# Kernel optimization log

Hardware: AMD Instinct MI355X
Metric: run time of the kernel (lower is better)

## Reference

```python
import jax, jax.numpy as jnp
import numpy as np

NUM_HEADS = 8
SPLIT = 2  # split_size; idx=0 -> H_sp=H, W_sp=SPLIT (horizontal stripes)


def setup_inputs() -> dict:
    key = jax.random.key(0)
    k1, k2, k3 = jax.random.split(key, 3)
    B, C, H, W = 4, 64, 128, 128
    temp = jax.random.normal(k1, (B, 3, C, H, W), dtype=jnp.float32)
    conv_w = jax.random.normal(k2, (C, 1, 3, 3), dtype=jnp.float32) * 0.1  # depthwise OIHW
    conv_b = jax.random.normal(k3, (C,), dtype=jnp.float32) * 0.1
    return {"temp": temp, "conv_w": conv_w, "conv_b": conv_b}


def reference(temp, conv_w, conv_b):
    B, _, C, H, W = temp.shape
    hd = C // NUM_HEADS
    scale = hd ** (-0.5)
    H_sp, W_sp = H, SPLIT  # idx == 0

    # symmetric pad to multiples of window size (faithful to original; zero here)
    H_pad = (H_sp - H % H_sp) % H_sp
    W_pad = (W_sp - W % W_sp) % W_sp
    top, left = H_pad // 2, W_pad // 2
    x = jnp.pad(temp, ((0, 0), (0, 0), (0, 0), (top, H_pad - top), (left, W_pad - left)))
    H_, W_ = H + H_pad, W + W_pad
    q, k, v = x[:, 0], x[:, 1], x[:, 2]  # each [B,C,H_,W_]

    nW = (H_ // H_sp) * (W_ // W_sp)
    N = H_sp * W_sp  # tokens per window

    def im2cswin(t):
        # [B,C,H_,W_] -> [B*nW, heads, N, hd]
        w = t.reshape(B, C, H_ // H_sp, H_sp, W_ // W_sp, W_sp)
        w = w.transpose(0, 2, 4, 3, 5, 1).reshape(-1, N, C)
        return w.reshape(-1, N, NUM_HEADS, hd).transpose(0, 2, 1, 3)

    qh = im2cswin(q) * scale
    kh = im2cswin(k)

    # v windows as images [B*nW, C, H_sp, W_sp] for depthwise LePE conv
    vw = v.reshape(B, C, H_ // H_sp, H_sp, W_ // W_sp, W_sp)
    vw = vw.transpose(0, 2, 4, 1, 3, 5).reshape(-1, C, H_sp, W_sp)
    rpe = jax.lax.conv_general_dilated(
        vw, conv_w, window_strides=(1, 1), padding='SAME',
        feature_group_count=C, dimension_numbers=('NCHW', 'OIHW', 'NCHW'))
    rpe = rpe + conv_b[None, :, None, None]

    vh = vw.reshape(-1, NUM_HEADS, hd, N).transpose(0, 1, 3, 2)    # [B*nW,h,N,hd]
    rpeh = rpe.reshape(-1, NUM_HEADS, hd, N).transpose(0, 1, 3, 2)

    attn = jax.nn.softmax(jnp.einsum('whnd,whmd->whnm', qh, kh), axis=-1)
    out = jnp.einsum('whnm,whmd->whnd', attn, vh) + rpeh           # [B*nW,h,N,hd]

    out = out.transpose(0, 2, 1, 3).reshape(-1, N, C)              # [B*nW,N,C]
    # windows2img + crop
    out = out.reshape(B, H_ // H_sp, W_ // W_sp, H_sp, W_sp, C)
    out = out.transpose(0, 1, 3, 2, 4, 5).reshape(B, H_, W_, C)
    out = out[:, top:H + top, left:W + left, :]
    return out.reshape(B, H * W, C)
```

## Files before the change

kernel.cpp:

```cpp
#include <hip/hip_runtime.h>
#include <hip/hip_bf16.h>
#include <stdint.h>


typedef __attribute__((ext_vector_type(4))) short bf16x4;
typedef __attribute__((ext_vector_type(4))) float f32x4;

static __device__ __forceinline__ uint32_t pk2(float x, float y) {
    union { __hip_bfloat162 h2; uint32_t u; } c;
    c.h2 = __float22bfloat162_rn(make_float2(x, y));
    return c.u;
}
static __device__ __forceinline__ float bflo(uint32_t u){ return __uint_as_float(u<<16); }
static __device__ __forceinline__ float bfhi(uint32_t u){ return __uint_as_float(u & 0xffff0000u); }

static __device__ __forceinline__ uint2 ld2(const char* p) {
    uint2 r;
    r.x = *(const uint32_t*)(p);
    r.y = *(const uint32_t*)(p + 4);
    return r;
}

static __device__ __forceinline__ f32x4 mfma16x16x16bf16(bf16x4 a, bf16x4 b, f32x4 c) {
#if __has_builtin(__builtin_amdgcn_mfma_f32_16x16x16bf16_1k)
    return __builtin_amdgcn_mfma_f32_16x16x16bf16_1k(a, b, c, 0, 0, 0);
#else
    f32x4 d;
    asm volatile("v_mfma_f32_16x16x16_bf16 %0, %1, %2, %3\n\ts_nop 7\n\ts_nop 7"
                 : "=v"(d) : "v"(a), "v"(b), "v"(c));
    return d;
#endif
}

#define QK_TOK_STR 20
#define QK_WIN_STR 5120
#define V_CH_STR   536
#define V_WIN_STR  4288

__global__ __launch_bounds__(512, 4)
void lepe_attn(const float* __restrict__ temp,
               const float* __restrict__ conv_w,
               const float* __restrict__ conv_b,
               float* __restrict__ out)
{
    __shared__ __align__(16) char smem[58432];
    char* q_s = smem;
    char* k_s = smem + 20480;
    char* v_t = smem + 40960;
    float* cw_s = (float*)(smem + 58112);

    const int tid  = threadIdx.x;
    const int wave = tid >> 6, lane = tid & 63;
    const int lr = lane & 15, quad = lane >> 4;
    const int win   = wave & 3;
    const int qbase = (wave >> 2) * 8;

    const int bid = blockIdx.x;
    const int x  = bid & 7;
    int t_ = bid >> 3;
    const int wjh  = t_ & 1;  t_ >>= 1;
    const int head = t_ & 7;
    const int b    = t_ >> 3;
    const int wi   = x*8 + wjh*4 + win;

    const size_t cstr = 16384, sstr = 64 * cstr;
    const float qs = 0.35355339059327373f * 1.4426950408889634f;

    {
        const int cg = wave;
        const int hg = lane >> 1, hf1 = lane & 1;
        const int w0 = hf1 * 2;
        const float* bp = temp + (size_t)b*3*sstr + (size_t)(head*8 + cg)*cstr
                        + x*16 + wjh*8 + hf1*4;
        #pragma unroll
        for (int i = 0; i < 4; ++i) {
            int h = i*32 + hg;
            float4 fq = *(const float4*)(bp + (size_t)h*128);
            uint32_t a0 = pk2(fq.x*qs, fq.y*qs);
            uint32_t a1 = pk2(fq.z*qs, fq.w*qs);
            *(uint16_t*)(q_s + w0*QK_WIN_STR     + (2*h)*QK_TOK_STR   + cg*2) = (uint16_t)a0;
            *(uint16_t*)(q_s + w0*QK_WIN_STR     + (2*h+1)*QK_TOK_STR + cg*2) = (uint16_t)(a0>>16);
            *(uint16_t*)(q_s + (w0+1)*QK_WIN_STR + (2*h)*QK_TOK_STR   + cg*2) = (uint16_t)a1;
            *(uint16_t*)(q_s + (w0+1)*QK_WIN_STR + (2*h+1)*QK_TOK_STR + cg*2) = (uint16_t)(a1>>16);
            float4 fk = *(const float4*)(bp + sstr + (size_t)h*128);
            uint32_t b0 = pk2(fk.x, fk.y);
            uint32_t b1 = pk2(fk.z, fk.w);
            *(uint16_t*)(k_s + w0*QK_WIN_STR     + (2*h)*QK_TOK_STR   + cg*2) = (uint16_t)b0;
            *(uint16_t*)(k_s + w0*QK_WIN_STR     + (2*h+1)*QK_TOK_STR + cg*2) = (uint16_t)(b0>>16);
            *(uint16_t*)(k_s + (w0+1)*QK_WIN_STR + (2*h)*QK_TOK_STR   + cg*2) = (uint16_t)b1;
            *(uint16_t*)(k_s + (w0+1)*QK_WIN_STR + (2*h+1)*QK_TOK_STR + cg*2) = (uint16_t)(b1>>16);
            float4 fv = *(const float4*)(bp + 2*sstr + (size_t)h*128);
            *(uint32_t*)(v_t + w0*V_WIN_STR     + cg*V_CH_STR + 4*h + 4) = pk2(fv.x, fv.y);
            *(uint32_t*)(v_t + (w0+1)*V_WIN_STR + cg*V_CH_STR + 4*h + 4) = pk2(fv.z, fv.w);
        }
        if (tid < 72) cw_s[tid] = conv_w[head*72 + tid];
        if (tid < 8)  cw_s[72 + tid] = conv_b[head*8 + tid];
        if (tid < 32) {
            int vw = tid >> 3, vc = tid & 7;
            *(uint32_t*)(v_t + vw*V_WIN_STR + vc*V_CH_STR)       = 0;
            *(uint32_t*)(v_t + vw*V_WIN_STR + vc*V_CH_STR + 516) = 0;
        }
    }
    __syncthreads();

    const f32x4 zf = {0.f, 0.f, 0.f, 0.f};
    const uint2 z2 = make_uint2(0, 0);
    uint2 kf[16]; uint2 vf[16];
    #pragma unroll
    for (int T = 0; T < 16; ++T) {
        uint2 kk = ld2(k_s + win*QK_WIN_STR + (T*16 + lr)*QK_TOK_STR + (quad & 1)*8);
        kf[T] = (quad < 2) ? kk : z2;
        uint2 vv = ld2(v_t + win*V_WIN_STR + (lane & 7)*V_CH_STR + 4 + (T*16 + quad*4)*2);
        vf[T] = (lr < 8) ? vv : z2;
    }
    __syncthreads();

    {
        const int w2  = tid >> 7;
        const int chl = (tid >> 4) & 7;
        const int seg = tid & 15;
        const char* base = v_t + w2*V_WIN_STR + chl*V_CH_STR + seg*32;
        uint32_t d[10];
        *(uint2*)(d+0) = *(const uint2*)(base);
        *(uint2*)(d+2) = *(const uint2*)(base+8);
        *(uint2*)(d+4) = *(const uint2*)(base+16);
        *(uint2*)(d+6) = *(const uint2*)(base+24);
        *(uint2*)(d+8) = *(const uint2*)(base+32);
        float w9[9];
        #pragma unroll
        for (int k = 0; k < 9; ++k) w9[k] = cw_s[chl*9 + k];
        const float bia = cw_s[72 + chl];
        #pragma unroll
        for (int tt = 0; tt < 16; ++tt) {
            int tok = seg*16 + tt;
            int w01 = tok & 1;
            int L = (tt >> 1) * 2;
            float rp = bia;
            #pragma unroll
            for (int dy = 0; dy < 3; ++dy) {
                #pragma unroll
                for (int wp = 0; wp < 2; ++wp) {
                    int idx = L + 2*dy + wp;
                    uint32_t dw = d[idx >> 1];
                    float tap = (idx & 1) ? bfhi(dw) : bflo(dw);
                    rp = fmaf(w9[dy*3 + wp + 1 - w01], tap, rp);
                }
            }
            union { __hip_bfloat16 h; uint16_t u; } cv;
            cv.h = __float2bfloat16(rp);
            *(uint16_t*)(k_s + w2*QK_WIN_STR + tok*QK_TOK_STR + chl*2) = cv.u;
        }
    }
    __syncthreads();

    #pragma unroll 1
    for (int qg0 = 0; qg0 < 8; ++qg0) {
        const int qg = qbase + qg0;
        uint2 qq = ld2(q_s + win*QK_WIN_STR + (qg*16 + lr)*QK_TOK_STR + (quad & 1)*8);
        union { uint2 u; bf16x4 h4; } qf; qf.u = (quad < 2) ? qq : z2;
        f32x4 acc = zf;
        float rsum = 0.f;
        #pragma unroll
        for (int T = 0; T < 16; ++T) {
            union { uint2 u; bf16x4 h4; } kfu; kfu.u = kf[T];
            f32x4 sc = mfma16x16x16bf16(kfu.h4, qf.h4, zf);
            float e0 = __builtin_amdgcn_exp2f(sc[0]);
            float e1 = __builtin_amdgcn_exp2f(sc[1]);
            float e2 = __builtin_amdgcn_exp2f(sc[2]);
            float e3 = __builtin_amdgcn_exp2f(sc[3]);
            rsum += (e0 + e1) + (e2 + e3);
            union { uint2 u; bf16x4 h4; } pb; pb.u = make_uint2(pk2(e0,e1), pk2(e2,e3));
            union { uint2 u; bf16x4 h4; } vfu; vfu.u = vf[T];
            acc = mfma16x16x16bf16(vfu.h4, pb.h4, acc);
        }
        float rs = rsum;
        rs += __shfl_xor(rs, 16);
        rs += __shfl_xor(rs, 32);
        const float rinv = __builtin_amdgcn_rcpf(rs);
        if (quad < 2) {
            int tok = qg*16 + lr;
            int h = tok >> 1, w01 = tok & 1;
            uint2 rp2 = ld2(k_s + win*QK_WIN_STR + tok*QK_TOK_STR + quad*8);
            float4 ov;
            ov.x = fmaf(acc[0], rinv, bflo(rp2.x));
            ov.y = fmaf(acc[1], rinv, bfhi(rp2.x));
            ov.z = fmaf(acc[2], rinv, bflo(rp2.y));
            ov.w = fmaf(acc[3], rinv, bfhi(rp2.y));
            size_t addr = (size_t)b*1048576 + (size_t)(h*128 + wi*2 + w01)*64
                        + head*8 + quad*4;
            *(float4*)(out + addr) = ov;
        }
    }
}

extern "C" void kernel_launch(void* const* d_in, const int* in_sizes, int n_in,
                              void* d_out, int out_size, void* d_ws, size_t ws_size,
                              hipStream_t stream) {
    const float* temp = (const float*)d_in[0];
    const float* cw   = (const float*)d_in[1];
    const float* cb   = (const float*)d_in[2];
    float* o = (float*)d_out;
    (void)in_sizes; (void)n_in; (void)out_size; (void)d_ws; (void)ws_size;
    lepe_attn<<<dim3(512), dim3(512), 0, stream>>>(temp, cw, cb, o);
}
```

Before: 115.4 us.

## Shrink LDS with XOR-swizzled Q/K layout and fold softmax sum into MFMA

```diff
diff --git a/kernel.cpp b/kernel.cpp
--- a/kernel.cpp
+++ b/kernel.cpp
@@ -19,6 +19,10 @@
     r.x = *(const uint32_t*)(p);
     r.y = *(const uint32_t*)(p + 4);
     return r;
+}
+
+static __device__ __forceinline__ int qk_off(int tok) {
+    return (tok * 16) ^ ((tok >> 4 & 7) << 4);
 }
 
 static __device__ __forceinline__ f32x4 mfma16x16x16bf16(bf16x4 a, bf16x4 b, f32x4 c) {
@@ -32,22 +36,21 @@
 #endif
 }
 
-#define QK_TOK_STR 20
-#define QK_WIN_STR 5120
+#define QK_WIN_STR 4128
 #define V_CH_STR   536
 #define V_WIN_STR  4288
 
-__global__ __launch_bounds__(512, 4)
+__global__ __launch_bounds__(512, 6)
 void lepe_attn(const float* __restrict__ temp,
                const float* __restrict__ conv_w,
                const float* __restrict__ conv_b,
                float* __restrict__ out)
 {
-    __shared__ __align__(16) char smem[58432];
+    __shared__ __align__(16) char smem[50496];
     char* q_s = smem;
-    char* k_s = smem + 20480;
-    char* v_t = smem + 40960;
-    float* cw_s = (float*)(smem + 58112);
+    char* k_s = smem + 16512;
+    char* v_t = smem + 33024;
+    float* cw_s = (float*)(smem + 50176);
 
     const int tid  = threadIdx.x;
     const int wave = tid >> 6, lane = tid & 63;
@@ -75,20 +78,21 @@
         #pragma unroll
         for (int i = 0; i < 4; ++i) {
             int h = i*32 + hg;
+            int o0 = qk_off(2*h), o1 = qk_off(2*h + 1);
             float4 fq = *(const float4*)(bp + (size_t)h*128);
             uint32_t a0 = pk2(fq.x*qs, fq.y*qs);
             uint32_t a1 = pk2(fq.z*qs, fq.w*qs);
-            *(uint16_t*)(q_s + w0*QK_WIN_STR     + (2*h)*QK_TOK_STR   + cg*2) = (uint16_t)a0;
-            *(uint16_t*)(q_s + w0*QK_WIN_STR     + (2*h+1)*QK_TOK_STR + cg*2) = (uint16_t)(a0>>16);
-            *(uint16_t*)(q_s + (w0+1)*QK_WIN_STR + (2*h)*QK_TOK_STR   + cg*2) = (uint16_t)a1;
-            *(uint16_t*)(q_s + (w0+1)*QK_WIN_STR + (2*h+1)*QK_TOK_STR + cg*2) = (uint16_t)(a1>>16);
+            *(uint16_t*)(q_s + w0*QK_WIN_STR     + o0 + cg*2) = (uint16_t)a0;
+            *(uint16_t*)(q_s + w0*QK_WIN_STR     + o1 + cg*2) = (uint16_t)(a0>>16);
+            *(uint16_t*)(q_s + (w0+1)*QK_WIN_STR + o0 + cg*2) = (uint16_t)a1;
+            *(uint16_t*)(q_s + (w0+1)*QK_WIN_STR + o1 + cg*2) = (uint16_t)(a1>>16);
             float4 fk = *(const float4*)(bp + sstr + (size_t)h*128);
             uint32_t b0 = pk2(fk.x, fk.y);
             uint32_t b1 = pk2(fk.z, fk.w);
-            *(uint16_t*)(k_s + w0*QK_WIN_STR     + (2*h)*QK_TOK_STR   + cg*2) = (uint16_t)b0;
-            *(uint16_t*)(k_s + w0*QK_WIN_STR     + (2*h+1)*QK_TOK_STR + cg*2) = (uint16_t)(b0>>16);
-            *(uint16_t*)(k_s + (w0+1)*QK_WIN_STR + (2*h)*QK_TOK_STR   + cg*2) = (uint16_t)b1;
-            *(uint16_t*)(k_s + (w0+1)*QK_WIN_STR + (2*h+1)*QK_TOK_STR + cg*2) = (uint16_t)(b1>>16);
+            *(uint16_t*)(k_s + w0*QK_WIN_STR     + o0 + cg*2) = (uint16_t)b0;
+            *(uint16_t*)(k_s + w0*QK_WIN_STR     + o1 + cg*2) = (uint16_t)(b0>>16);
+            *(uint16_t*)(k_s + (w0+1)*QK_WIN_STR + o0 + cg*2) = (uint16_t)b1;
+            *(uint16_t*)(k_s + (w0+1)*QK_WIN_STR + o1 + cg*2) = (uint16_t)(b1>>16);
             float4 fv = *(const float4*)(bp + 2*sstr + (size_t)h*128);
             *(uint32_t*)(v_t + w0*V_WIN_STR     + cg*V_CH_STR + 4*h + 4) = pk2(fv.x, fv.y);
             *(uint32_t*)(v_t + (w0+1)*V_WIN_STR + cg*V_CH_STR + 4*h + 4) = pk2(fv.z, fv.w);
@@ -105,13 +109,14 @@
 
     const f32x4 zf = {0.f, 0.f, 0.f, 0.f};
     const uint2 z2 = make_uint2(0, 0);
+    const uint2 ones2 = make_uint2(0x3F803F80u, 0x3F803F80u);
     uint2 kf[16]; uint2 vf[16];
     #pragma unroll
     for (int T = 0; T < 16; ++T) {
-        uint2 kk = ld2(k_s + win*QK_WIN_STR + (T*16 + lr)*QK_TOK_STR + (quad & 1)*8);
+        uint2 kk = ld2(k_s + win*QK_WIN_STR + qk_off(T*16 + lr) + (quad & 1)*8);
         kf[T] = (quad < 2) ? kk : z2;
         uint2 vv = ld2(v_t + win*V_WIN_STR + (lane & 7)*V_CH_STR + 4 + (T*16 + quad*4)*2);
-        vf[T] = (lr < 8) ? vv : z2;
+        vf[T] = (lr < 8) ? vv : ((lr == 8) ? ones2 : z2);
     }
     __syncthreads();
 
@@ -148,7 +153,7 @@
             }
             union { __hip_bfloat16 h; uint16_t u; } cv;
             cv.h = __float2bfloat16(rp);
-            *(uint16_t*)(k_s + w2*QK_WIN_STR + tok*QK_TOK_STR + chl*2) = cv.u;
+            *(uint16_t*)(k_s + w2*QK_WIN_STR + qk_off(tok) + chl*2) = cv.u;
         }
     }
     __syncthreads();
@@ -156,10 +161,9 @@
     #pragma unroll 1
     for (int qg0 = 0; qg0 < 8; ++qg0) {
         const int qg = qbase + qg0;
-        uint2 qq = ld2(q_s + win*QK_WIN_STR + (qg*16 + lr)*QK_TOK_STR + (quad & 1)*8);
+        uint2 qq = ld2(q_s + win*QK_WIN_STR + qk_off(qg*16 + lr) + (quad & 1)*8);
         union { uint2 u; bf16x4 h4; } qf; qf.u = (quad < 2) ? qq : z2;
         f32x4 acc = zf;
-        float rsum = 0.f;
         #pragma unroll
         for (int T = 0; T < 16; ++T) {
             union { uint2 u; bf16x4 h4; } kfu; kfu.u = kf[T];
@@ -168,19 +172,16 @@
             float e1 = __builtin_amdgcn_exp2f(sc[1]);
             float e2 = __builtin_amdgcn_exp2f(sc[2]);
             float e3 = __builtin_amdgcn_exp2f(sc[3]);
-            rsum += (e0 + e1) + (e2 + e3);
             union { uint2 u; bf16x4 h4; } pb; pb.u = make_uint2(pk2(e0,e1), pk2(e2,e3));
             union { uint2 u; bf16x4 h4; } vfu; vfu.u = vf[T];
             acc = mfma16x16x16bf16(vfu.h4, pb.h4, acc);
         }
-        float rs = rsum;
-        rs += __shfl_xor(rs, 16);
-        rs += __shfl_xor(rs, 32);
+        float rs = __shfl(acc[0], 32 + lr);
         const float rinv = __builtin_amdgcn_rcpf(rs);
         if (quad < 2) {
             int tok = qg*16 + lr;
             int h = tok >> 1, w01 = tok & 1;
-            uint2 rp2 = ld2(k_s + win*QK_WIN_STR + tok*QK_TOK_STR + quad*8);
+            uint2 rp2 = ld2(k_s + win*QK_WIN_STR + qk_off(tok) + quad*8);
             float4 ov;
             ov.x = fmaf(acc[0], rinv, bflo(rp2.x));
             ov.y = fmaf(acc[1], rinv, bfhi(rp2.x));
```

After: 132.3 us. 1.15x slower.
